# Kernel tuning notes

Measured on AMD Instinct MI355X. Metric: run time of the kernel, lower is better.

## Reference

```python
import jax, jax.numpy as jnp
import numpy as np

B, DIM, H, W = 8, 192, 128, 128
HEADS, WIN, SHIFT, MLP = 6, 8, 4, 4
EPS = 1e-5


def _rel_pos_index():
    w = WIN
    coords = np.stack(np.meshgrid(np.arange(w), np.arange(w), indexing='ij'))  # [2,w,w]
    cf = coords.reshape(2, -1)
    rel = cf[:, :, None] - cf[:, None, :]  # [2,N,N]
    rel = rel.transpose(1, 2, 0).astype(np.int64)
    rel[..., 0] += w - 1
    rel[..., 1] += w - 1
    rel[..., 0] *= 2 * w - 1
    return rel.sum(-1)  # [N,N]


def _attn_mask():
    # standard Swin shifted-window mask, -100 on cross-region pairs
    w, s = WIN, SHIFT
    img = np.zeros((H, W), np.float32)
    cnt = 0
    for hs in (slice(0, -w), slice(-w, -s), slice(-s, None)):
        for ws in (slice(0, -w), slice(-w, -s), slice(-s, None)):
            img[hs, ws] = cnt
            cnt += 1
    mw = img.reshape(H // w, w, W // w, w).transpose(0, 2, 1, 3).reshape(-1, w * w)
    am = mw[:, None, :] - mw[:, :, None]
    return np.where(am != 0, -100.0, 0.0).astype(np.float32)  # [nW,N,N]


def _layernorm(x, wgt, b):
    mu = x.mean(-1, keepdims=True)
    var = jnp.mean((x - mu) ** 2, -1, keepdims=True)
    return (x - mu) * jax.lax.rsqrt(var + EPS) * wgt + b


def setup_inputs() -> dict:
    C, hid = DIM, MLP * DIM
    k = jax.random.split(jax.random.key(0), 8)
    s = 0.02
    f32 = jnp.float32
    return {
        'x': jax.random.normal(k[0], (B, C, H, W), f32),
        'gn_w': jnp.ones((C,), f32), 'gn_b': jnp.zeros((C,), f32),
        'ln1_w': jnp.ones((C,), f32), 'ln1_b': jnp.zeros((C,), f32),
        'qkv_w': jax.random.normal(k[1], (C, 3 * C), f32) * s,
        'qkv_b': jnp.zeros((3 * C,), f32),
        'proj_w': jax.random.normal(k[2], (C, C), f32) * s,
        'proj_b': jnp.zeros((C,), f32),
        'rpb': jax.random.normal(k[3], ((2 * WIN - 1) ** 2, HEADS), f32) * s,
        'ln2_w': jnp.ones((C,), f32), 'ln2_b': jnp.zeros((C,), f32),
        'fc1_w': jax.random.normal(k[4], (C, hid), f32) * s,
        'fc1_b': jnp.zeros((hid,), f32),
        'fc2_w': jax.random.normal(k[5], (hid, C), f32) * s,
        'fc2_b': jnp.zeros((C,), f32),
    }


def reference(x, gn_w, gn_b, ln1_w, ln1_b, qkv_w, qkv_b, proj_w, proj_b, rpb,
              ln2_w, ln2_b, fc1_w, fc1_b, fc2_w, fc2_b):
    Bb, C, Hh, Ww = x.shape
    w, s, nh = WIN, SHIFT, HEADS
    hd = C // nh
    N = w * w
    # GroupNorm(1, C): normalize over (C,H,W) per sample
    mu = x.mean((1, 2, 3), keepdims=True)
    var = jnp.mean((x - mu) ** 2, (1, 2, 3), keepdims=True)
    xg = (x - mu) * jax.lax.rsqrt(var + EPS)
    xg = xg * gn_w[None, :, None, None] + gn_b[None, :, None, None]
    xb = jnp.transpose(xg, (0, 2, 3, 1))  # [B,H,W,C]
    residual = xb
    # --- SwinTransformerBlock ---
    shortcut = xb
    h = _layernorm(xb, ln1_w, ln1_b)
    h = jnp.roll(h, (-s, -s), axis=(1, 2))  # cyclic shift
    # window partition -> [B*nW, N, C]
    hw = h.reshape(Bb, Hh // w, w, Ww // w, w, C).transpose(0, 1, 3, 2, 4, 5).reshape(-1, N, C)
    qkv = (hw @ qkv_w + qkv_b).reshape(-1, N, 3, nh, hd).transpose(2, 0, 3, 1, 4)
    q, k_, v = qkv[0], qkv[1], qkv[2]  # [B*nW, nh, N, hd]
    attn = (q * (hd ** -0.5)) @ jnp.swapaxes(k_, -2, -1)  # [B*nW, nh, N, N]
    bias = rpb[jnp.asarray(_rel_pos_index().reshape(-1))].reshape(N, N, nh).transpose(2, 0, 1)
    attn = attn + bias[None]
    mask = jnp.asarray(_attn_mask())  # [nW,N,N]
    nW = mask.shape[0]
    attn = attn.reshape(Bb, nW, nh, N, N) + mask[None, :, None, :, :]
    attn = jax.nn.softmax(attn.reshape(-1, nh, N, N), axis=-1)
    out = jnp.swapaxes(attn @ v, 1, 2).reshape(-1, N, C)
    out = out @ proj_w + proj_b
    # window reverse + reverse shift
    out = out.reshape(Bb, Hh // w, Ww // w, w, w, C).transpose(0, 1, 3, 2, 4, 5).reshape(Bb, Hh, Ww, C)
    out = jnp.roll(out, (s, s), axis=(1, 2))
    xb = shortcut + out
    m = jax.nn.gelu(_layernorm(xb, ln2_w, ln2_b) @ fc1_w + fc1_b, approximate=False)
    xb = xb + (m @ fc2_w + fc2_b)
    # --- wrapper residual + clamp ---
    y = jnp.transpose(xb + residual, (0, 3, 1, 2))
    return jnp.clip(y, -10.0, 10.0)
```

## Files before the change

kernel.cpp:

```cpp
#include <hip/hip_runtime.h>
#include <cstddef>

typedef __attribute__((ext_vector_type(8))) short bf16x8;
typedef __attribute__((ext_vector_type(4))) float f32x4;
typedef __attribute__((ext_vector_type(4))) short s16x4;

#define DEV __device__ __forceinline__
#define MFMA16(a,b,c) __builtin_amdgcn_mfma_f32_16x16x32_bf16((a),(b),(c),0,0,0)

DEV unsigned short f2bf(float f){
  unsigned int x = __float_as_uint(f);
  x += 0x7fffu + ((x >> 16) & 1u);
  return (unsigned short)(x >> 16);
}
DEV unsigned int pack2(float a, float b){
  return (unsigned int)f2bf(a) | ((unsigned int)f2bf(b) << 16);
}
DEV float gelu_f(float x){
  float z = fabsf(x) * 0.7071067811865475f;
  float tt = 1.f / (1.f + 0.3275911f * z);
  float poly = tt*(0.254829592f + tt*(-0.284496736f + tt*(1.421413741f +
               tt*(-1.453152027f + tt*1.061405429f))));
  float er = 1.f - poly * __expf(-z*z);
  er = (x < 0.f) ? -er : er;
  return 0.5f * x * (1.f + er);
}

__global__ void transpose_cast_all(const float* __restrict__ qkvw, const float* __restrict__ projw,
                                   const float* __restrict__ fc1w, const float* __restrict__ fc2w,
                                   unsigned short* __restrict__ qkvB, unsigned short* __restrict__ projB,
                                   unsigned short* __restrict__ fc1B, unsigned short* __restrict__ fc2B){
  int blk = blockIdx.x;
  const float* in; unsigned short* outp; int K, N, idx;
  if (blk < 432){        in = qkvw; outp = qkvB; K = 192; N = 576; idx = blk*256 + threadIdx.x; }
  else if (blk < 576){   in = projw; outp = projB; K = 192; N = 192; idx = (blk-432)*256 + threadIdx.x; }
  else if (blk < 1152){  in = fc1w; outp = fc1B; K = 192; N = 768; idx = (blk-576)*256 + threadIdx.x; }
  else {                 in = fc2w; outp = fc2B; K = 768; N = 192; idx = (blk-1152)*256 + threadIdx.x; }
  if (idx < K * N){
    int n = idx / K, k = idx - n * K;
    outp[idx] = f2bf(in[k * N + n]);
  }
}

__global__ void gn_partial(const float* __restrict__ x, float* __restrict__ part){
  int bc = blockIdx.x, tid = threadIdx.x;
  const float4* p = (const float4*)(x + (size_t)bc * 16384);
  float s = 0.f, s2 = 0.f;
  for (int i = tid; i < 4096; i += 256){
    float4 v = p[i];
    s  += v.x + v.y + v.z + v.w;
    s2 += v.x*v.x + v.y*v.y + v.z*v.z + v.w*v.w;
  }
  #pragma unroll
  for (int off = 32; off; off >>= 1){ s += __shfl_down(s, off); s2 += __shfl_down(s2, off); }
  __shared__ float red[8];
  int wid = tid >> 6;
  if ((tid & 63) == 0){ red[wid*2] = s; red[wid*2+1] = s2; }
  __syncthreads();
  if (tid == 0){
    part[bc*2]   = red[0] + red[2] + red[4] + red[6];
    part[bc*2+1] = red[1] + red[3] + red[5] + red[7];
  }
}

__global__ void gn_final(const float* __restrict__ part, float* __restrict__ stats){
  int b = blockIdx.x, tid = threadIdx.x;
  float s = 0.f, s2 = 0.f;
  for (int c = tid; c < 192; c += 64){
    s  += part[(b*192 + c)*2];
    s2 += part[(b*192 + c)*2 + 1];
  }
  #pragma unroll
  for (int off = 32; off; off >>= 1){ s += __shfl_down(s, off); s2 += __shfl_down(s2, off); }
  if (tid == 0){
    const float inv = 1.f / (192.f * 16384.f);
    float mean = s * inv;
    float var  = s2 * inv - mean*mean;
    stats[b*2]   = mean;
    stats[b*2+1] = rsqrtf(var + 1e-5f);
  }
}

__global__ void gn_apply(const float* __restrict__ x, const float* __restrict__ stats,
                         const float* __restrict__ gnw, const float* __restrict__ gnb,
                         float* __restrict__ xb){
  __shared__ float tile[192*64];
  int blk = blockIdx.x, tid = threadIdx.x;
  int b = blk >> 8, p0 = (blk & 255) * 64;
  float mean = stats[b*2], rstd = stats[b*2+1];
  #pragma unroll 1
  for (int i = 0; i < 12; i++){
    int idx4 = i*256 + tid;
    int c = idx4 >> 4, pq = idx4 & 15;
    float4 v = *(const float4*)(x + (((size_t)b*192 + c) << 14) + p0 + pq*4);
    float w  = gnw[c] * rstd;
    float bb = gnb[c] - mean * rstd * gnw[c];
    int pb_ = pq*4;
    tile[c*64 + ((pb_     + c) & 63)] = v.x * w + bb;
    tile[c*64 + ((pb_ + 1 + c) & 63)] = v.y * w + bb;
    tile[c*64 + ((pb_ + 2 + c) & 63)] = v.z * w + bb;
    tile[c*64 + ((pb_ + 3 + c) & 63)] = v.w * w + bb;
  }
  __syncthreads();
  #pragma unroll 1
  for (int i = 0; i < 12; i++){
    int idx4 = i*256 + tid;
    int pix = idx4 / 48, c4 = idx4 - pix*48;
    int cb = c4 * 4;
    float4 o;
    o.x = tile[(cb  )*64 + ((pix + cb    ) & 63)];
    o.y = tile[(cb+1)*64 + ((pix + cb + 1) & 63)];
    o.z = tile[(cb+2)*64 + ((pix + cb + 2) & 63)];
    o.w = tile[(cb+3)*64 + ((pix + cb + 3) & 63)];
    *(float4*)(xb + ((size_t)blk*64 + pix)*192 + cb) = o;
  }
}

__launch_bounds__(256, 3)
__global__ void attn_kernel(const float* __restrict__ xb, float* __restrict__ xb2,
                            const float* __restrict__ ln1w, const float* __restrict__ ln1b,
                            const unsigned short* __restrict__ qkvB, const float* __restrict__ qkvb,
                            const unsigned short* __restrict__ projB, const float* __restrict__ projb,
                            const float* __restrict__ rpb){
  __shared__ __align__(16) unsigned char smem[49408];
  int* regions = (int*)(smem + 49152);

  const int tid = threadIdx.x;
  const int blk = blockIdx.x;
  const int b = blk >> 8, wloc = blk & 255, wh = wloc >> 4, ww = wloc & 15;
  const int lane = tid & 63, wv = tid >> 6;
  const int ln15 = lane & 15, l16 = lane >> 4;
  const f32x4 zero4 = {0.f, 0.f, 0.f, 0.f};

  const int t = tid >> 2, q4 = tid & 3, c0 = q4 * 48;
  const int tr = t >> 3, tc = t & 7;
  const int sh = (wh*8 + tr + 4) & 127, sw = (ww*8 + tc + 4) & 127;
  const float* xrow = xb + (size_t)((((b << 7) + sh) << 7) + sw) * 192;
  float lnm, lnr;
  const int hswz = (t & 7) << 4;

  {
    float4 xt[12];
    float s = 0.f, s2 = 0.f;
    #pragma unroll
    for (int i = 0; i < 12; i++){
      xt[i] = *(const float4*)(xrow + c0 + i*4);
      s  += xt[i].x + xt[i].y + xt[i].z + xt[i].w;
      s2 += xt[i].x*xt[i].x + xt[i].y*xt[i].y + xt[i].z*xt[i].z + xt[i].w*xt[i].w;
    }
    s  += __shfl_xor(s, 1);  s  += __shfl_xor(s, 2);
    s2 += __shfl_xor(s2, 1); s2 += __shfl_xor(s2, 2);
    lnm = s * (1.f/192.f);
    lnr = rsqrtf(s2 * (1.f/192.f) - lnm*lnm + 1e-5f);
    #pragma unroll
    for (int i = 0; i < 12; i++){
      int cb = c0 + i*4;
      float4 w4 = *(const float4*)(ln1w + cb);
      float4 b4 = *(const float4*)(ln1b + cb);
      uint2 u;
      u.x = pack2((xt[i].x - lnm)*lnr*w4.x + b4.x, (xt[i].y - lnm)*lnr*w4.y + b4.y);
      u.y = pack2((xt[i].z - lnm)*lnr*w4.z + b4.z, (xt[i].w - lnm)*lnr*w4.w + b4.w);
      *(uint2*)(smem + t*384 + ((cb*2) ^ hswz)) = u;
    }
    if (q4 == 0){
      int gh = wh*8 + tr, gw = ww*8 + tc;
      regions[t] = (gh < 120 ? 0 : (gh < 124 ? 1 : 2)) * 3 + (gw < 120 ? 0 : (gw < 124 ? 1 : 2));
    }
  }
  __syncthreads();

  f32x4 pacc[4][3];
  #pragma unroll
  for (int mt = 0; mt < 4; mt++)
    #pragma unroll
    for (int nt = 0; nt < 3; nt++)
      pacc[mt][nt] = zero4;

  const float scale = 0.17677669529663687f;

  #pragma unroll 1
  for (int hp = 0; hp < 3; hp++){
    const int h0 = hp * 2;
    if (hp){
      __syncthreads();
      #pragma unroll 2
      for (int i = 0; i < 12; i++){
        int cb = c0 + i*4;
        float4 xi = *(const float4*)(xrow + cb);
        float4 w4 = *(const float4*)(ln1w + cb);
        float4 b4 = *(const float4*)(ln1b + cb);
        uint2 u;
        u.x = pack2((xi.x - lnm)*lnr*w4.x + b4.x, (xi.y - lnm)*lnr*w4.y + b4.y);
        u.y = pack2((xi.z - lnm)*lnr*w4.z + b4.z, (xi.w - lnm)*lnr*w4.w + b4.w);
        *(uint2*)(smem + t*384 + ((cb*2) ^ hswz)) = u;
      }
      __syncthreads();
    }

    #pragma unroll 1
    for (int tt0 = 0; tt0 < 3; tt0++){
      const int tt = wv*3 + tt0;
      const int which = tt >> 2, sub = tt & 3;
      const int colb = which*192 + h0*32 + sub*16;
      const unsigned short* bp = qkvB + (size_t)(colb + ln15)*192 + l16*8;
      bf16x8 bw[6];
      #pragma unroll
      for (int ks = 0; ks < 6; ks++) bw[ks] = *(const bf16x8*)(bp + ks*32);
      f32x4 acc[4];
      #pragma unroll
      for (int mt = 0; mt < 4; mt++){
        acc[mt] = zero4;
        const int arow = mt*16 + ln15;
        const unsigned char* ap = smem + arow*384;
        const int aswz = (arow & 7) << 4;
        #pragma unroll
        for (int ks = 0; ks < 6; ks++){
          bf16x8 af = *(const bf16x8*)(ap + ((ks*64 + l16*16) ^ aswz));
          acc[mt] = MFMA16(af, bw[ks], acc[mt]);
        }
      }
      const float bias = qkvb[colb + ln15];
      const int local = sub*16 + ln15;
      const int hl = local >> 5, d = local & 31;
      if (which == 2){
        unsigned char* vbase = smem + 40960 + hl*4096 + d*128;
        const int vswz = (d & 7) << 4;
        #pragma unroll
        for (int mt = 0; mt < 4; mt++){
          const int tk2 = (mt*16 + l16*4) * 2;
          *(unsigned int*)(vbase + ((tk2    ) ^ vswz)) = pack2(acc[mt][0] + bias, acc[mt][1] + bias);
          *(unsigned int*)(vbase + ((tk2 + 4) ^ vswz)) = pack2(acc[mt][2] + bias, acc[mt][3] + bias);
        }
      } else {
        unsigned char* qkb = smem + 24576 + hl*8192;
        const int koff = which ? 64 : 0;
        const float mul = which ? 1.f : scale;
        #pragma unroll
        for (int mt = 0; mt < 4; mt++)
          #pragma unroll
          for (int reg = 0; reg < 4; reg++){
            const int tok = mt*16 + l16*4 + reg;
            *(unsigned short*)(qkb + tok*128 + ((koff + d*2) ^ ((tok & 7) << 4))) =
                f2bf((acc[mt][reg] + bias) * mul);
          }
      }
    }
    __syncthreads();

    #pragma unroll 1
    for (int e = 0; e < 2; e++){
      const int h = h0 + e;
      const unsigned char* qkb = smem + 24576 + e*8192;
      const int arow = wv*16 + ln15;
      const int aswz = (arow & 7) << 4;
      bf16x8 aq = *(const bf16x8*)(qkb + arow*128 + ((l16*16) ^ aswz));
      f32x4 sacc[4];
      #pragma unroll
      for (int nt = 0; nt < 4; nt++){
        const int brow = nt*16 + ln15;
        bf16x8 bk = *(const bf16x8*)(qkb + brow*128 + ((64 + l16*16) ^ ((brow & 7) << 4)));
        sacc[nt] = MFMA16(aq, bk, zero4);
      }
      #pragma unroll
      for (int nt = 0; nt < 4; nt++){
        const int j_tok = nt*16 + ln15;
        const int rj = j_tok >> 3, cj = j_tok & 7;
        const int regj = regions[j_tok];
        #pragma unroll
        for (int reg = 0; reg < 4; reg++){
          const int i_tok = wv*16 + l16*4 + reg;
          const int ri = i_tok >> 3, ci = i_tok & 7;
          float bias = rpb[((ri - rj + 7)*15 + (ci - cj + 7))*6 + h];
          sacc[nt][reg] += bias + ((regions[i_tok] == regj) ? 0.f : -100.f);
        }
      }
      float mx[4], sum[4];
      #pragma unroll
      for (int reg = 0; reg < 4; reg++){
        float m = fmaxf(fmaxf(sacc[0][reg], sacc[1][reg]), fmaxf(sacc[2][reg], sacc[3][reg]));
        m = fmaxf(m, __shfl_xor(m, 1));
        m = fmaxf(m, __shfl_xor(m, 2));
        m = fmaxf(m, __shfl_xor(m, 4));
        m = fmaxf(m, __shfl_xor(m, 8));
        mx[reg] = m; sum[reg] = 0.f;
      }
      #pragma unroll
      for (int nt = 0; nt < 4; nt++)
        #pragma unroll
        for (int reg = 0; reg < 4; reg++){
          float ex = __expf(sacc[nt][reg] - mx[reg]);
          sacc[nt][reg] = ex;
          sum[reg] += ex;
        }
      #pragma unroll
      for (int reg = 0; reg < 4; reg++){
        float sm = sum[reg];
        sm += __shfl_xor(sm, 1);
        sm += __shfl_xor(sm, 2);
        sm += __shfl_xor(sm, 4);
        sm += __shfl_xor(sm, 8);
        sum[reg] = 1.f / sm;
      }
      #pragma unroll
      for (int nt = 0; nt < 4; nt++)
        #pragma unroll
        for (int reg = 0; reg < 4; reg++){
          const int tok = wv*16 + l16*4 + reg;
          *(unsigned short*)(smem + tok*128 + (((nt*16 + ln15)*2) ^ ((tok & 7) << 4))) =
              f2bf(sacc[nt][reg] * sum[reg]);
        }
      f32x4 cacc[2] = {zero4, zero4};
      #pragma unroll
      for (int ks = 0; ks < 2; ks++){
        bf16x8 pa = *(const bf16x8*)(smem + arow*128 + ((ks*64 + l16*16) ^ aswz));
        #pragma unroll
        for (int nt2 = 0; nt2 < 2; nt2++){
          const int drow = nt2*16 + ln15;
          bf16x8 bv = *(const bf16x8*)(smem + 40960 + e*4096 + drow*128 +
                                       ((ks*64 + l16*16) ^ ((drow & 7) << 4)));
          cacc[nt2] = MFMA16(pa, bv, cacc[nt2]);
        }
      }
      #pragma unroll
      for (int nt2 = 0; nt2 < 2; nt2++)
        #pragma unroll
        for (int reg = 0; reg < 4; reg++){
          const int tok = wv*16 + l16*4 + reg;
          const int col = e*32 + nt2*16 + ln15;
          *(unsigned short*)(smem + 8192 + tok*128 + ((col*2) ^ ((tok & 7) << 4))) =
              f2bf(cacc[nt2][reg]);
        }
    }
    __syncthreads();

    #pragma unroll
    for (int ks = 0; ks < 2; ks++){
      bf16x8 bw3[3];
      #pragma unroll
      for (int nt3 = 0; nt3 < 3; nt3++)
        bw3[nt3] = *(const bf16x8*)(projB + (size_t)(wv*48 + nt3*16 + ln15)*192 + h0*32 + ks*32 + l16*8);
      #pragma unroll
      for (int mt = 0; mt < 4; mt++){
        const int crow = mt*16 + ln15;
        bf16x8 ac = *(const bf16x8*)(smem + 8192 + crow*128 + ((ks*64 + l16*16) ^ ((crow & 7) << 4)));
        #pragma unroll
        for (int nt3 = 0; nt3 < 3; nt3++)
          pacc[mt][nt3] = MFMA16(ac, bw3[nt3], pacc[mt][nt3]);
      }
    }
  }
  __syncthreads();

  #pragma unroll
  for (int nt3 = 0; nt3 < 3; nt3++){
    const int col4 = (wv*48 + nt3*16 + ln15) * 4;
    #pragma unroll
    for (int mt = 0; mt < 4; mt++)
      #pragma unroll
      for (int reg = 0; reg < 4; reg++){
        const int row = mt*16 + l16*4 + reg;
        *(float*)(smem + row*768 + (col4 ^ ((row & 7) << 4))) = pacc[mt][nt3][reg];
      }
  }
  __syncthreads();
  {
    #pragma unroll
    for (int i = 0; i < 12; i++){
      const int id = i*256 + tid;
      const int tok = id / 48, c4 = id - tok*48;
      const int trr = tok >> 3, tcc = tok & 7;
      const int shh = (wh*8 + trr + 4) & 127, sww = (ww*8 + tcc + 4) & 127;
      const size_t goff = ((size_t)((((b << 7) + shh) << 7) + sww)) * 192 + c4*4;
      float4 pv  = *(const float4*)(smem + tok*768 + ((c4*16) ^ ((tok & 7) << 4)));
      float4 xr  = *(const float4*)(xb + goff);
      float4 pb4 = *(const float4*)(projb + c4*4);
      float4 o;
      o.x = xr.x + pv.x + pb4.x;
      o.y = xr.y + pv.y + pb4.y;
      o.z = xr.z + pv.z + pb4.z;
      o.w = xr.w + pv.w + pb4.w;
      *(float4*)(xb2 + goff) = o;
    }
  }
}

__launch_bounds__(256, 3)
__global__ void mlp_kernel(const float* __restrict__ xb, float* __restrict__ xb2,
                           const float* __restrict__ ln2w, const float* __restrict__ ln2b,
                           const unsigned short* __restrict__ fc1B, const float* __restrict__ fc1b,
                           const unsigned short* __restrict__ fc2B, const float* __restrict__ fc2b,
                           float* __restrict__ outp, const int fuse){
  __shared__ __align__(16) unsigned char smem[49152];

  const int tid = threadIdx.x;
  const int lane = tid & 63, wv = tid >> 6;
  const int ln15 = lane & 15, l16 = lane >> 4;
  const size_t p0 = (size_t)blockIdx.x * 64;
  const f32x4 zero4 = {0.f, 0.f, 0.f, 0.f};

  const int t = tid >> 2, q4 = tid & 3, c0 = q4 * 48;
  const int hswz = (t & 7) << 4;
  const float* xrow2 = xb2 + (p0 + t)*192;

  {
    float4 xt[12];
    float s = 0.f, s2 = 0.f;
    #pragma unroll
    for (int i = 0; i < 12; i++){
      xt[i] = *(const float4*)(xrow2 + c0 + i*4);
      s  += xt[i].x + xt[i].y + xt[i].z + xt[i].w;
      s2 += xt[i].x*xt[i].x + xt[i].y*xt[i].y + xt[i].z*xt[i].z + xt[i].w*xt[i].w;
    }
    s  += __shfl_xor(s, 1);  s  += __shfl_xor(s, 2);
    s2 += __shfl_xor(s2, 1); s2 += __shfl_xor(s2, 2);
    const float mean = s * (1.f/192.f);
    const float rstd = rsqrtf(s2 * (1.f/192.f) - mean*mean + 1e-5f);
    #pragma unroll
    for (int i = 0; i < 12; i++){
      int cb = c0 + i*4;
      float4 w4 = *(const float4*)(ln2w + cb);
      float4 b4 = *(const float4*)(ln2b + cb);
      uint2 u;
      u.x = pack2((xt[i].x - mean)*rstd*w4.x + b4.x, (xt[i].y - mean)*rstd*w4.y + b4.y);
      u.y = pack2((xt[i].z - mean)*rstd*w4.z + b4.z, (xt[i].w - mean)*rstd*w4.w + b4.w);
      *(uint2*)(smem + t*384 + ((cb*2) ^ hswz)) = u;
    }
  }
  __syncthreads();

  f32x4 o2[4][3];
  #pragma unroll
  for (int mt = 0; mt < 4; mt++)
    #pragma unroll
    for (int nt = 0; nt < 3; nt++)
      o2[mt][nt] = zero4;

  {
    const unsigned short* bp1 = fc1B + (size_t)(wv*16 + ln15)*192 + l16*8;
    bf16x8 w1[6];
    #pragma unroll
    for (int ks = 0; ks < 6; ks++) w1[ks] = *(const bf16x8*)(bp1 + ks*32);
    const float4 b1 = *(const float4*)(fc1b + wv*16 + l16*4);
    unsigned char* hb = smem + 24576;
    #pragma unroll
    for (int mt = 0; mt < 4; mt++){
      f32x4 facc = zero4;
      const int arow = mt*16 + ln15;
      const unsigned char* ap = smem + arow*384;
      const int aswz = (arow & 7) << 4;
      #pragma unroll
      for (int ks = 0; ks < 6; ks++){
        bf16x8 af = *(const bf16x8*)(ap + ((ks*64 + l16*16) ^ aswz));
        facc = MFMA16(w1[ks], af, facc);
      }
      s16x4 hv;
      hv.x = (short)f2bf(gelu_f(facc[0] + b1.x));
      hv.y = (short)f2bf(gelu_f(facc[1] + b1.y));
      hv.z = (short)f2bf(gelu_f(facc[2] + b1.z));
      hv.w = (short)f2bf(gelu_f(facc[3] + b1.w));
      *(s16x4*)(hb + arow*128 + ((wv*32 + l16*8) ^ aswz)) = hv;
    }
  }
  __syncthreads();

  #pragma unroll 1
  for (int ch = 1; ch < 12; ch++){
    bf16x8 w2[3][2];
    #pragma unroll
    for (int nt3 = 0; nt3 < 3; nt3++)
      #pragma unroll
      for (int ks = 0; ks < 2; ks++)
        w2[nt3][ks] = *(const bf16x8*)(fc2B + (size_t)(wv*48 + nt3*16 + ln15)*768 +
                                       (ch-1)*64 + ks*32 + l16*8);
    const unsigned short* bp1 = fc1B + (size_t)(ch*64 + wv*16 + ln15)*192 + l16*8;
    bf16x8 w1[6];
    #pragma unroll
    for (int ks = 0; ks < 6; ks++) w1[ks] = *(const bf16x8*)(bp1 + ks*32);
    const float4 b1 = *(const float4*)(fc1b + ch*64 + wv*16 + l16*4);

    {
      const unsigned char* hb = smem + 24576 + ((ch-1)&1)*8192;
      #pragma unroll
      for (int mt = 0; mt < 4; mt++){
        const int brow = mt*16 + ln15;
        const unsigned char* bp = hb + brow*128;
        const int bswz = (brow & 7) << 4;
        #pragma unroll
        for (int ks = 0; ks < 2; ks++){
          bf16x8 hf = *(const bf16x8*)(bp + ((ks*64 + l16*16) ^ bswz));
          #pragma unroll
          for (int nt3 = 0; nt3 < 3; nt3++)
            o2[mt][nt3] = MFMA16(w2[nt3][ks], hf, o2[mt][nt3]);
        }
      }
    }
    {
      unsigned char* hb = smem + 24576 + (ch&1)*8192;
      #pragma unroll
      for (int mt = 0; mt < 4; mt++){
        f32x4 facc = zero4;
        const int arow = mt*16 + ln15;
        const unsigned char* ap = smem + arow*384;
        const int aswz = (arow & 7) << 4;
        #pragma unroll
        for (int ks = 0; ks < 6; ks++){
          bf16x8 af = *(const bf16x8*)(ap + ((ks*64 + l16*16) ^ aswz));
          facc = MFMA16(w1[ks], af, facc);
        }
        s16x4 hv;
        hv.x = (short)f2bf(gelu_f(facc[0] + b1.x));
        hv.y = (short)f2bf(gelu_f(facc[1] + b1.y));
        hv.z = (short)f2bf(gelu_f(facc[2] + b1.z));
        hv.w = (short)f2bf(gelu_f(facc[3] + b1.w));
        *(s16x4*)(hb + arow*128 + ((wv*32 + l16*8) ^ aswz)) = hv;
      }
    }
    __syncthreads();
  }

  {
    bf16x8 w2[3][2];
    #pragma unroll
    for (int nt3 = 0; nt3 < 3; nt3++)
      #pragma unroll
      for (int ks = 0; ks < 2; ks++)
        w2[nt3][ks] = *(const bf16x8*)(fc2B + (size_t)(wv*48 + nt3*16 + ln15)*768 +
                                       11*64 + ks*32 + l16*8);
    const unsigned char* hb = smem + 24576 + 8192;
    #pragma unroll
    for (int mt = 0; mt < 4; mt++){
      const int brow = mt*16 + ln15;
      const unsigned char* bp = hb + brow*128;
      const int bswz = (brow & 7) << 4;
      #pragma unroll
      for (int ks = 0; ks < 2; ks++){
        bf16x8 hf = *(const bf16x8*)(bp + ((ks*64 + l16*16) ^ bswz));
        #pragma unroll
        for (int nt3 = 0; nt3 < 3; nt3++)
          o2[mt][nt3] = MFMA16(w2[nt3][ks], hf, o2[mt][nt3]);
      }
    }
  }
  __syncthreads();

  #pragma unroll
  for (int mt = 0; mt < 4; mt++){
    const int tok = mt*16 + ln15;
    const int tswz = (tok & 7) << 4;
    unsigned char* rp = smem + tok*768;
    #pragma unroll
    for (int nt3 = 0; nt3 < 3; nt3++){
      const int cb = wv*192 + nt3*64 + l16*16;
      *(f32x4*)(rp + (cb ^ tswz)) = o2[mt][nt3];
    }
  }
  __syncthreads();

  const float* xrow = xb + (p0 + t)*192;
  if (!fuse){
    float* orow = xb2 + (p0 + t)*192;
    #pragma unroll
    for (int i = 0; i < 12; i++){
      float4 mv  = *(const float4*)(smem + t*768 + ((c0*4 + i*16) ^ hswz));
      float4 x2  = *(const float4*)(xrow2 + c0 + i*4);
      float4 xr  = *(const float4*)(xrow + c0 + i*4);
      float4 fb4 = *(const float4*)(fc2b + c0 + i*4);
      float4 o;
      o.x = x2.x + xr.x + fb4.x + mv.x;
      o.y = x2.y + xr.y + fb4.y + mv.y;
      o.z = x2.z + xr.z + fb4.z + mv.z;
      o.w = x2.w + xr.w + fb4.w + mv.w;
      *(float4*)(orow + c0 + i*4) = o;
    }
  } else {
    #pragma unroll
    for (int i = 0; i < 12; i++){
      const int off = (c0*4 + i*16) ^ hswz;
      float4 mv  = *(const float4*)(smem + t*768 + off);
      float4 x2  = *(const float4*)(xrow2 + c0 + i*4);
      float4 xr  = *(const float4*)(xrow + c0 + i*4);
      float4 fb4 = *(const float4*)(fc2b + c0 + i*4);
      float4 o;
      o.x = fminf(fmaxf(x2.x + xr.x + fb4.x + mv.x, -10.f), 10.f);
      o.y = fminf(fmaxf(x2.y + xr.y + fb4.y + mv.y, -10.f), 10.f);
      o.z = fminf(fmaxf(x2.z + xr.z + fb4.z + mv.z, -10.f), 10.f);
      o.w = fminf(fmaxf(x2.w + xr.w + fb4.w + mv.w, -10.f), 10.f);
      *(float4*)(smem + t*768 + off) = o;
    }
    __syncthreads();
    const int bidx   = (int)(p0 >> 14);
    const int imgoff = (int)(p0 & 16383);
    #pragma unroll 1
    for (int i = 0; i < 12; i++){
      const int id = i*256 + tid;
      const int c = id >> 4, pq = id & 15;
      float4 o4;
      o4.x = *(const float*)(smem + (pq*4    )*768 + ((c*4) ^ (((pq*4    ) & 7) << 4)));
      o4.y = *(const float*)(smem + (pq*4 + 1)*768 + ((c*4) ^ (((pq*4 + 1) & 7) << 4)));
      o4.z = *(const float*)(smem + (pq*4 + 2)*768 + ((c*4) ^ (((pq*4 + 2) & 7) << 4)));
      o4.w = *(const float*)(smem + (pq*4 + 3)*768 + ((c*4) ^ (((pq*4 + 3) & 7) << 4)));
      *(float4*)(outp + (((size_t)(bidx*192 + c)) << 14) + imgoff + pq*4) = o4;
    }
  }
}

__global__ void final_k(const float* __restrict__ xb2, float* __restrict__ out){
  __shared__ float tile[192*64];
  int blk = blockIdx.x, tid = threadIdx.x;
  int b = blk >> 8, p0 = (blk & 255) * 64;
  #pragma unroll 1
  for (int i = 0; i < 12; i++){
    int idx4 = i*256 + tid;
    int tt = idx4 / 48, c4 = idx4 - tt*48;
    int cb = c4 * 4;
    float4 v = *(const float4*)(xb2 + ((size_t)blk*64 + tt)*192 + cb);
    tile[(cb  )*64 + ((tt + cb    ) & 63)] = v.x;
    tile[(cb+1)*64 + ((tt + cb + 1) & 63)] = v.y;
    tile[(cb+2)*64 + ((tt + cb + 2) & 63)] = v.z;
    tile[(cb+3)*64 + ((tt + cb + 3) & 63)] = v.w;
  }
  __syncthreads();
  #pragma unroll 1
  for (int i = 0; i < 12; i++){
    int idx4 = i*256 + tid;
    int c = idx4 >> 4, pq = idx4 & 15;
    int pb_ = pq*4;
    float4 o;
    o.x = tile[c*64 + ((pb_     + c) & 63)];
    o.y = tile[c*64 + ((pb_ + 1 + c) & 63)];
    o.z = tile[c*64 + ((pb_ + 2 + c) & 63)];
    o.w = tile[c*64 + ((pb_ + 3 + c) & 63)];
    o.x = fminf(fmaxf(o.x, -10.f), 10.f);
    o.y = fminf(fmaxf(o.y, -10.f), 10.f);
    o.z = fminf(fmaxf(o.z, -10.f), 10.f);
    o.w = fminf(fmaxf(o.w, -10.f), 10.f);
    *(float4*)(out + (((size_t)b*192 + c) << 14) + p0 + pb_) = o;
  }
}

extern "C" void kernel_launch(void* const* d_in, const int* in_sizes, int n_in,
                              void* d_out, int out_size, void* d_ws, size_t ws_size,
                              hipStream_t stream){
  (void)in_sizes; (void)n_in; (void)out_size;
  const float* x     = (const float*)d_in[0];
  const float* gnw   = (const float*)d_in[1];
  const float* gnb   = (const float*)d_in[2];
  const float* ln1w  = (const float*)d_in[3];
  const float* ln1b  = (const float*)d_in[4];
  const float* qkvw  = (const float*)d_in[5];
  const float* qkvb  = (const float*)d_in[6];
  const float* projw = (const float*)d_in[7];
  const float* projb = (const float*)d_in[8];
  const float* rpb   = (const float*)d_in[9];
  const float* ln2w  = (const float*)d_in[10];
  const float* ln2b  = (const float*)d_in[11];
  const float* fc1w  = (const float*)d_in[12];
  const float* fc1b  = (const float*)d_in[13];
  const float* fc2w  = (const float*)d_in[14];
  const float* fc2b  = (const float*)d_in[15];
  float* out = (float*)d_out;

  float* ws    = (float*)d_ws;
  float* xb2   = ws;
  float* part  = xb2  + 25165824;
  float* stats = part + 3072;
  unsigned short* qkvB = (unsigned short*)(stats + 16);
  unsigned short* projB = qkvB + 110592;
  unsigned short* fc1B  = projB + 36864;
  unsigned short* fc2B  = fc1B + 147456;

  const int fuse = (ws_size >= 202223680ULL) ? 1 : 0;
  float* xb = fuse ? (ws + 25390096) : out;

  transpose_cast_all<<<1728, 256, 0, stream>>>(qkvw, projw, fc1w, fc2w, qkvB, projB, fc1B, fc2B);
  gn_partial<<<1536, 256, 0, stream>>>(x, part);
  gn_final<<<8, 64, 0, stream>>>(part, stats);
  gn_apply<<<2048, 256, 0, stream>>>(x, stats, gnw, gnb, xb);
  attn_kernel<<<2048, 256, 0, stream>>>(xb, xb2, ln1w, ln1b, qkvB, qkvb, projB, projb, rpb);
  mlp_kernel<<<2048, 256, 0, stream>>>(xb, xb2, ln2w, ln2b, fc1B, fc1b, fc2B, fc2b, out, fuse);
  if (!fuse) final_k<<<2048, 256, 0, stream>>>(xb2, out);
}
```

Measured before the change: 814.5 us.

## Split attention kernel into QKV+attention kernel and separate projection kernel

Splits the fused window-attention kernel in two. The first does LayerNorm, the QKV projection and per-head attention in head pairs, then writes the bf16 context to a global scratch buffer. The second does the output projection plus the residual add. The split is meant to lower per-kernel register and shared-memory pressure and improve scheduling. In exchange it adds a global round trip for the context tensor and one extra launch, and it only runs when the workspace is large enough.

Measured after the change: 670.7 us. -17.7%, faster.

```diff
diff --git a/kernel.cpp b/kernel.cpp
--- a/kernel.cpp
+++ b/kernel.cpp
@@ -24,6 +24,10 @@
   float er = 1.f - poly * __expf(-z*z);
   er = (x < 0.f) ? -er : er;
   return 0.5f * x * (1.f + er);
+}
+DEV int region_of(int tok, int wh, int ww){
+  int gh = wh*8 + (tok >> 3), gw = ww*8 + (tok & 7);
+  return (gh < 120 ? 0 : (gh < 124 ? 1 : 2)) * 3 + (gw < 120 ? 0 : (gw < 124 ? 1 : 2));
 }
 
 __global__ void transpose_cast_all(const float* __restrict__ qkvw, const float* __restrict__ projw,
@@ -116,6 +120,291 @@
   }
 }
 
+__launch_bounds__(256, 2)
+__global__ void attn_qkv_kernel(const float* __restrict__ xb, unsigned short* __restrict__ ctxg,
+                                const float* __restrict__ ln1w, const float* __restrict__ ln1b,
+                                const unsigned short* __restrict__ qkvB, const float* __restrict__ qkvb,
+                                const float* __restrict__ rpb){
+  __shared__ __align__(16) unsigned char smem[65536];
+
+  const int tid = threadIdx.x;
+  const int blk = blockIdx.x;
+  const int b = blk >> 8, wloc = blk & 255, wh = wloc >> 4, ww = wloc & 15;
+  const int lane = tid & 63, wv = tid >> 6;
+  const int ln15 = lane & 15, l16 = lane >> 4;
+  const f32x4 zero4 = {0.f, 0.f, 0.f, 0.f};
+
+  const int t = tid >> 2, q4 = tid & 3, c0 = q4 * 48;
+  const int tr = t >> 3, tc = t & 7;
+  const int sh = (wh*8 + tr + 4) & 127, sw = (ww*8 + tc + 4) & 127;
+  const float* xrow = xb + (size_t)((((b << 7) + sh) << 7) + sw) * 192;
+  const int hswz = (t & 7) << 4;
+
+  {
+    float4 xt[12];
+    float s = 0.f, s2 = 0.f;
+    #pragma unroll
+    for (int i = 0; i < 12; i++){
+      xt[i] = *(const float4*)(xrow + c0 + i*4);
+      s  += xt[i].x + xt[i].y + xt[i].z + xt[i].w;
+      s2 += xt[i].x*xt[i].x + xt[i].y*xt[i].y + xt[i].z*xt[i].z + xt[i].w*xt[i].w;
+    }
+    s  += __shfl_xor(s, 1);  s  += __shfl_xor(s, 2);
+    s2 += __shfl_xor(s2, 1); s2 += __shfl_xor(s2, 2);
+    const float lnm = s * (1.f/192.f);
+    const float lnr = rsqrtf(s2 * (1.f/192.f) - lnm*lnm + 1e-5f);
+    #pragma unroll
+    for (int i = 0; i < 12; i++){
+      int cb = c0 + i*4;
+      float4 w4 = *(const float4*)(ln1w + cb);
+      float4 b4 = *(const float4*)(ln1b + cb);
+      uint2 u;
+      u.x = pack2((xt[i].x - lnm)*lnr*w4.x + b4.x, (xt[i].y - lnm)*lnr*w4.y + b4.y);
+      u.y = pack2((xt[i].z - lnm)*lnr*w4.z + b4.z, (xt[i].w - lnm)*lnr*w4.w + b4.w);
+      *(uint2*)(smem + t*384 + ((cb*2) ^ hswz)) = u;
+    }
+  }
+  __syncthreads();
+
+  const float scale = 0.17677669529663687f;
+
+  int regi[4], regj[4];
+  #pragma unroll
+  for (int r = 0; r < 4; r++) regi[r] = region_of(wv*16 + l16*4 + r, wh, ww);
+  #pragma unroll
+  for (int nt = 0; nt < 4; nt++) regj[nt] = region_of(nt*16 + ln15, wh, ww);
+
+  #pragma unroll 1
+  for (int hp = 0; hp < 3; hp++){
+    const int h0 = hp * 2;
+
+    #pragma unroll 1
+    for (int tt0 = 0; tt0 < 3; tt0++){
+      const int tt = wv*3 + tt0;
+      const int which = tt >> 2, sub = tt & 3;
+      const int colb = which*192 + h0*32 + sub*16;
+      const unsigned short* bp = qkvB + (size_t)(colb + ln15)*192 + l16*8;
+      bf16x8 bw[6];
+      #pragma unroll
+      for (int ks = 0; ks < 6; ks++) bw[ks] = *(const bf16x8*)(bp + ks*32);
+      f32x4 acc[4];
+      #pragma unroll
+      for (int mt = 0; mt < 4; mt++){
+        acc[mt] = zero4;
+        const int arow = mt*16 + ln15;
+        const unsigned char* ap = smem + arow*384;
+        const int aswz = (arow & 7) << 4;
+        #pragma unroll
+        for (int ks = 0; ks < 6; ks++){
+          bf16x8 af = *(const bf16x8*)(ap + ((ks*64 + l16*16) ^ aswz));
+          acc[mt] = MFMA16(af, bw[ks], acc[mt]);
+        }
+      }
+      const float bias = qkvb[colb + ln15];
+      const int local = sub*16 + ln15;
+      const int hl = local >> 5, d = local & 31;
+      if (which == 2){
+        unsigned char* vbase = smem + 49152 + hl*4096 + d*128;
+        const int vswz = (d & 7) << 4;
+        #pragma unroll
+        for (int mt = 0; mt < 4; mt++){
+          const int tk2 = (mt*16 + l16*4) * 2;
+          *(unsigned int*)(vbase + ((tk2    ) ^ vswz)) = pack2(acc[mt][0] + bias, acc[mt][1] + bias);
+          *(unsigned int*)(vbase + ((tk2 + 4) ^ vswz)) = pack2(acc[mt][2] + bias, acc[mt][3] + bias);
+        }
+      } else {
+        unsigned char* qkb = smem + 32768 + hl*8192;
+        const int koff = which ? 64 : 0;
+        const float mul = which ? 1.f : scale;
+        #pragma unroll
+        for (int mt = 0; mt < 4; mt++)
+          #pragma unroll
+          for (int reg = 0; reg < 4; reg++){
+            const int tok = mt*16 + l16*4 + reg;
+            *(unsigned short*)(qkb + tok*128 + ((koff + d*2) ^ ((tok & 7) << 4))) =
+                f2bf((acc[mt][reg] + bias) * mul);
+          }
+      }
+    }
+    __syncthreads();
+
+    #pragma unroll 1
+    for (int e = 0; e < 2; e++){
+      const int h = h0 + e;
+      const unsigned char* qkb = smem + 32768 + e*8192;
+      const int arow = wv*16 + ln15;
+      const int aswz = (arow & 7) << 4;
+      bf16x8 aq = *(const bf16x8*)(qkb + arow*128 + ((l16*16) ^ aswz));
+      f32x4 sacc[4];
+      #pragma unroll
+      for (int nt = 0; nt < 4; nt++){
+        const int brow = nt*16 + ln15;
+        bf16x8 bk = *(const bf16x8*)(qkb + brow*128 + ((64 + l16*16) ^ ((brow & 7) << 4)));
+        sacc[nt] = MFMA16(aq, bk, zero4);
+      }
+      #pragma unroll
+      for (int nt = 0; nt < 4; nt++){
+        const int j_tok = nt*16 + ln15;
+        const int rj = j_tok >> 3, cj = j_tok & 7;
+        #pragma unroll
+        for (int reg = 0; reg < 4; reg++){
+          const int i_tok = wv*16 + l16*4 + reg;
+          const int ri = i_tok >> 3, ci = i_tok & 7;
+          float bias = rpb[((ri - rj + 7)*15 + (ci - cj + 7))*6 + h];
+          sacc[nt][reg] += bias + ((regi[reg] == regj[nt]) ? 0.f : -100.f);
+        }
+      }
+      float mx[4], sum[4];
+      #pragma unroll
+      for (int reg = 0; reg < 4; reg++){
+        float m = fmaxf(fmaxf(sacc[0][reg], sacc[1][reg]), fmaxf(sacc[2][reg], sacc[3][reg]));
+        m = fmaxf(m, __shfl_xor(m, 1));
+        m = fmaxf(m, __shfl_xor(m, 2));
+        m = fmaxf(m, __shfl_xor(m, 4));
+        m = fmaxf(m, __shfl_xor(m, 8));
+        mx[reg] = m; sum[reg] = 0.f;
+      }
+      #pragma unroll
+      for (int nt = 0; nt < 4; nt++)
+        #pragma unroll
+        for (int reg = 0; reg < 4; reg++){
+          float ex = __expf(sacc[nt][reg] - mx[reg]);
+          sacc[nt][reg] = ex;
+          sum[reg] += ex;
+        }
+      #pragma unroll
+      for (int reg = 0; reg < 4; reg++){
+        float sm = sum[reg];
+        sm += __shfl_xor(sm, 1);
+        sm += __shfl_xor(sm, 2);
+        sm += __shfl_xor(sm, 4);
+        sm += __shfl_xor(sm, 8);
+        sum[reg] = 1.f / sm;
+      }
+      #pragma unroll
+      for (int nt = 0; nt < 4; nt++)
+        #pragma unroll
+        for (int reg = 0; reg < 4; reg++){
+          const int tok = wv*16 + l16*4 + reg;
+          *(unsigned short*)(smem + 57344 + tok*128 + (((nt*16 + ln15)*2) ^ ((tok & 7) << 4))) =
+              f2bf(sacc[nt][reg] * sum[reg]);
+        }
+      f32x4 cacc[2] = {zero4, zero4};
+      #pragma unroll
+      for (int ks = 0; ks < 2; ks++){
+        bf16x8 pa = *(const bf16x8*)(smem + 57344 + arow*128 + ((ks*64 + l16*16) ^ aswz));
+        #pragma unroll
+        for (int nt2 = 0; nt2 < 2; nt2++){
+          const int drow = nt2*16 + ln15;
+          bf16x8 bv = *(const bf16x8*)(smem + 49152 + e*4096 + drow*128 +
+                                       ((ks*64 + l16*16) ^ ((drow & 7) << 4)));
+          cacc[nt2] = MFMA16(pa, bv, cacc[nt2]);
+        }
+      }
+      #pragma unroll
+      for (int nt2 = 0; nt2 < 2; nt2++)
+        #pragma unroll
+        for (int reg = 0; reg < 4; reg++){
+          const int tok = wv*16 + l16*4 + reg;
+          const int col = e*32 + nt2*16 + ln15;
+          *(unsigned short*)(smem + 24576 + tok*128 + ((col*2) ^ ((tok & 7) << 4))) =
+              f2bf(cacc[nt2][reg]);
+        }
+    }
+    __syncthreads();
+
+    {
+      const int tok = tid >> 2, part = tid & 3;
+      const int s = (tok & 7) << 4;
+      bf16x8 v0 = *(const bf16x8*)(smem + 24576 + tok*128 + ((part*32     ) ^ s));
+      bf16x8 v1 = *(const bf16x8*)(smem + 24576 + tok*128 + ((part*32 + 16) ^ s));
+      unsigned short* dst = ctxg + (size_t)(blk*64 + tok)*192 + hp*64 + part*16;
+      *(bf16x8*)(dst    ) = v0;
+      *(bf16x8*)(dst + 8) = v1;
+    }
+  }
+}
+
+__launch_bounds__(256, 3)
+__global__ void proj_kernel(const unsigned short* __restrict__ ctxg, const float* __restrict__ xb,
+                            float* __restrict__ xb2,
+                            const unsigned short* __restrict__ projB, const float* __restrict__ projb){
+  __shared__ __align__(16) unsigned char smem[49152];
+
+  const int tid = threadIdx.x;
+  const int blk = blockIdx.x;
+  const int b = blk >> 8, wloc = blk & 255, wh = wloc >> 4, ww = wloc & 15;
+  const int lane = tid & 63, wv = tid >> 6;
+  const int ln15 = lane & 15, l16 = lane >> 4;
+  const f32x4 zero4 = {0.f, 0.f, 0.f, 0.f};
+
+  const int t = tid >> 2, q4 = tid & 3;
+  const int hswz = (t & 7) << 4;
+
+  {
+    const unsigned short* crow = ctxg + (size_t)(blk*64 + t)*192;
+    #pragma unroll
+    for (int j = 0; j < 6; j++){
+      bf16x8 v = *(const bf16x8*)(crow + q4*48 + j*8);
+      *(bf16x8*)(smem + t*384 + ((q4*96 + j*16) ^ hswz)) = v;
+    }
+  }
+  __syncthreads();
+
+  f32x4 acc[4][3];
+  #pragma unroll
+  for (int mt = 0; mt < 4; mt++)
+    #pragma unroll
+    for (int nt = 0; nt < 3; nt++)
+      acc[mt][nt] = zero4;
+
+  #pragma unroll 1
+  for (int ks = 0; ks < 6; ks++){
+    bf16x8 bw3[3];
+    #pragma unroll
+    for (int nt3 = 0; nt3 < 3; nt3++)
+      bw3[nt3] = *(const bf16x8*)(projB + (size_t)(wv*48 + nt3*16 + ln15)*192 + ks*32 + l16*8);
+    #pragma unroll
+    for (int mt = 0; mt < 4; mt++){
+      const int brow = mt*16 + ln15;
+      bf16x8 cf = *(const bf16x8*)(smem + brow*384 + ((ks*64 + l16*16) ^ ((brow & 7) << 4)));
+      #pragma unroll
+      for (int nt3 = 0; nt3 < 3; nt3++)
+        acc[mt][nt3] = MFMA16(bw3[nt3], cf, acc[mt][nt3]);
+    }
+  }
+  __syncthreads();
+
+  #pragma unroll
+  for (int mt = 0; mt < 4; mt++){
+    const int tok = mt*16 + ln15;
+    const int tswz = (tok & 7) << 4;
+    unsigned char* rp = smem + tok*768;
+    #pragma unroll
+    for (int nt3 = 0; nt3 < 3; nt3++)
+      *(f32x4*)(rp + ((wv*192 + nt3*64 + l16*16) ^ tswz)) = acc[mt][nt3];
+  }
+  __syncthreads();
+
+  #pragma unroll
+  for (int i = 0; i < 12; i++){
+    const int id = i*256 + tid;
+    const int tok = id / 48, c4 = id - tok*48;
+    const int trr = tok >> 3, tcc = tok & 7;
+    const int shh = (wh*8 + trr + 4) & 127, sww = (ww*8 + tcc + 4) & 127;
+    const size_t goff = ((size_t)((((b << 7) + shh) << 7) + sww)) * 192 + c4*4;
+    float4 pv  = *(const float4*)(smem + tok*768 + ((c4*16) ^ ((tok & 7) << 4)));
+    float4 xr  = *(const float4*)(xb + goff);
+    float4 pb4 = *(const float4*)(projb + c4*4);
+    float4 o;
+    o.x = xr.x + pv.x + pb4.x;
+    o.y = xr.y + pv.y + pb4.y;
+    o.z = xr.z + pv.z + pb4.z;
+    o.w = xr.w + pv.w + pb4.w;
+    *(float4*)(xb2 + goff) = o;
+  }
+}
+
 __launch_bounds__(256, 3)
 __global__ void attn_kernel(const float* __restrict__ xb, float* __restrict__ xb2,
                             const float* __restrict__ ln1w, const float* __restrict__ ln1b,
@@ -549,10 +838,8 @@
     const int tswz = (tok & 7) << 4;
     unsigned char* rp = smem + tok*768;
     #pragma unroll
-    for (int nt3 = 0; nt3 < 3; nt3++){
-      const int cb = wv*192 + nt3*64 + l16*16;
-      *(f32x4*)(rp + (cb ^ tswz)) = o2[mt][nt3];
-    }
+    for (int nt3 = 0; nt3 < 3; nt3++)
+      *(f32x4*)(rp + ((wv*192 + nt3*64 + l16*16) ^ tswz)) = o2[mt][nt3];
   }
   __syncthreads();
 
@@ -669,14 +956,20 @@
   unsigned short* fc1B  = projB + 36864;
   unsigned short* fc2B  = fc1B + 147456;
 
-  const int fuse = (ws_size >= 202223680ULL) ? 1 : 0;
-  float* xb = fuse ? (ws + 25390096) : out;
+  const int mode = (ws_size >= 252555328ULL) ? 2 : ((ws_size >= 202223680ULL) ? 1 : 0);
+  float* xb = (mode >= 1) ? (ws + 25390096) : out;
+  unsigned short* ctxg = (unsigned short*)(ws + 50555920);
 
   transpose_cast_all<<<1728, 256, 0, stream>>>(qkvw, projw, fc1w, fc2w, qkvB, projB, fc1B, fc2B);
   gn_partial<<<1536, 256, 0, stream>>>(x, part);
   gn_final<<<8, 64, 0, stream>>>(part, stats);
   gn_apply<<<2048, 256, 0, stream>>>(x, stats, gnw, gnb, xb);
-  attn_kernel<<<2048, 256, 0, stream>>>(xb, xb2, ln1w, ln1b, qkvB, qkvb, projB, projb, rpb);
-  mlp_kernel<<<2048, 256, 0, stream>>>(xb, xb2, ln2w, ln2b, fc1B, fc1b, fc2B, fc2b, out, fuse);
-  if (!fuse) final_k<<<2048, 256, 0, stream>>>(xb2, out);
-}
+  if (mode == 2){
+    attn_qkv_kernel<<<2048, 256, 0, stream>>>(xb, ctxg, ln1w, ln1b, qkvB, qkvb, rpb);
+    proj_kernel<<<2048, 256, 0, stream>>>(ctxg, xb, xb2, projB, projb);
+  } else {
+    attn_kernel<<<2048, 256, 0, stream>>>(xb, xb2, ln1w, ln1b, qkvB, qkvb, projB, projb, rpb);
+  }
+  mlp_kernel<<<2048, 256, 0, stream>>>(xb, xb2, ln2w, ln2b, fc1B, fc1b, fc2B, fc2b, out, mode >= 1);
+  if (mode == 0) final_k<<<2048, 256, 0, stream>>>(xb2, out);
+}
```
